# Performance work log

Hardware: AMD Instinct MI355X
Metric: run time of the kernel (lower is better)

The kernel has to match this reference:

```python
import jax, jax.numpy as jnp
import numpy as np

D_MODEL, N_HEADS, N_KV, HEAD_DIM, D_LAT = 1024, 8, 2, 128, 32
N_REP = N_HEADS // N_KV  # 4
B, T = 2, 2048


def setup_inputs() -> dict:
    key = jax.random.key(0)
    ks = jax.random.split(key, 8)
    s = lambda fan_in: 1.0 / np.sqrt(fan_in)
    return {
        "x": jax.random.normal(ks[0], (B, T, D_MODEL), jnp.float32),
        # weights stored as [in, out] (transpose of torch Linear.weight)
        "wq": jax.random.normal(ks[1], (D_MODEL, N_HEADS * HEAD_DIM), jnp.float32) * s(D_MODEL),
        "wk_down": jax.random.normal(ks[2], (D_MODEL, N_KV * D_LAT), jnp.float32) * s(D_MODEL),
        "wv_down": jax.random.normal(ks[3], (D_MODEL, N_KV * D_LAT), jnp.float32) * s(D_MODEL),
        "wk_up": jax.random.normal(ks[4], (D_LAT, HEAD_DIM), jnp.float32) * s(D_LAT),
        "wv_up": jax.random.normal(ks[5], (D_LAT, HEAD_DIM), jnp.float32) * s(D_LAT),
        "wo": jax.random.normal(ks[6], (N_HEADS * HEAD_DIM, D_MODEL), jnp.float32) * s(N_HEADS * HEAD_DIM),
    }


def reference(x, wq, wk_down, wv_down, wk_up, wv_up, wo):
    Bq, Tq, _ = x.shape
    scale = HEAD_DIM ** -0.5  # SDPA default scale
    # Q: [B,T,Hkv,Rep,Dh] (grouped view avoids materializing repeated K/V)
    q = (x @ wq).reshape(Bq, Tq, N_KV, N_REP, HEAD_DIM)
    # latent KV: [B,T,Hkv,Dl] -> up-project to [B,T,Hkv,Dh]
    k_lat = (x @ wk_down).reshape(Bq, Tq, N_KV, D_LAT)
    v_lat = (x @ wv_down).reshape(Bq, Tq, N_KV, D_LAT)
    k = jnp.einsum("bkhl,ld->bkhd", k_lat, wk_up)
    v = jnp.einsum("bkhl,ld->bkhd", v_lat, wv_up)
    # causal attention, GQA via grouped einsum (no repeat_interleave copy)
    scores = jnp.einsum("bqhrd,bkhd->bhrqk", q, k) * scale  # [B,Hkv,Rep,T,T]
    causal = jnp.tril(jnp.ones((Tq, Tq), dtype=bool))
    scores = jnp.where(causal, scores, jnp.finfo(scores.dtype).min)
    probs = jax.nn.softmax(scores, axis=-1)
    y = jnp.einsum("bhrqk,bkhd->bqhrd", probs, v)  # [B,T,Hkv,Rep,Dh]
    y = y.reshape(Bq, Tq, N_HEADS * HEAD_DIM)
    return y @ wo
```

## Files before the change

### kernel.cpp

```cpp
#include <hip/hip_runtime.h>
#include <hip/hip_bf16.h>


typedef __bf16 bf16_t;
typedef bf16_t bf16x8 __attribute__((ext_vector_type(8)));
typedef float f32x4 __attribute__((ext_vector_type(4)));

__device__ inline bf16x8 cvt8(const float* __restrict__ p) {
  f32x4 a = *(const f32x4*)p, b = *(const f32x4*)(p + 4);
  bf16x8 r;
#pragma unroll
  for (int i = 0; i < 4; ++i) { r[i] = (bf16_t)a[i]; r[4 + i] = (bf16_t)b[i]; }
  return r;
}

__global__ __launch_bounds__(256) void prep_mfma(
    const float* __restrict__ wq, const float* __restrict__ wkd,
    const float* __restrict__ wvd, const float* __restrict__ wku,
    const float* __restrict__ wvu, const float* __restrict__ wo,
    bf16_t* __restrict__ WqkvT, bf16_t* __restrict__ WcombT) {
  __shared__ __align__(16) char smem[34816];
  const int tid = threadIdx.x;
  const int wave = tid >> 6, lane = tid & 63;
  const int quad = lane >> 4, col = lane & 15;
  const int bi = blockIdx.x;

  if (bi < 64) {
    const int h = bi >> 3;
    const int c0 = (bi & 7) * 128 + wave * 32;
    f32x4 acc[2][2];
#pragma unroll
    for (int i = 0; i < 2; ++i)
#pragma unroll
      for (int j = 0; j < 2; ++j) acc[i][j] = (f32x4){0.f, 0.f, 0.f, 0.f};
#pragma unroll
    for (int ks = 0; ks < 4; ++ks) {
      const int ko = ks * 32 + quad * 8;
      bf16x8 a0 = cvt8(wku + col * 128 + ko);
      bf16x8 a1 = cvt8(wku + (16 + col) * 128 + ko);
      bf16x8 b0 = cvt8(wq + (size_t)(c0 + col) * 1024 + h * 128 + ko);
      bf16x8 b1 = cvt8(wq + (size_t)(c0 + 16 + col) * 1024 + h * 128 + ko);
      acc[0][0] = __builtin_amdgcn_mfma_f32_16x16x32_bf16(a0, b0, acc[0][0], 0, 0, 0);
      acc[0][1] = __builtin_amdgcn_mfma_f32_16x16x32_bf16(a0, b1, acc[0][1], 0, 0, 0);
      acc[1][0] = __builtin_amdgcn_mfma_f32_16x16x32_bf16(a1, b0, acc[1][0], 0, 0, 0);
      acc[1][1] = __builtin_amdgcn_mfma_f32_16x16x32_bf16(a1, b1, acc[1][1], 0, 0, 0);
    }
#pragma unroll
    for (int ms = 0; ms < 2; ++ms)
#pragma unroll
      for (int ns = 0; ns < 2; ++ns)
#pragma unroll
        for (int v = 0; v < 4; ++v)
          WqkvT[(size_t)(h * 32 + ms * 16 + quad * 4 + v) * 1024 + c0 + ns * 16 + col] =
              (bf16_t)acc[ms][ns][v];
  } else if (bi < 128) {
    const int b2 = bi - 64;
    const int h = b2 >> 3, m0 = (b2 & 7) * 128;
    bf16_t(*B_lds)[136] = (bf16_t(*)[136])smem;
    {
      const int d = tid >> 1, mh = (tid & 1) * 64;
      const float* wp = wo + (size_t)(h * 128 + d) * 1024 + m0 + mh;
#pragma unroll
      for (int i = 0; i < 16; ++i) {
        f32x4 w4 = *(const f32x4*)(wp + i * 4);
#pragma unroll
        for (int t = 0; t < 4; ++t) B_lds[mh + i * 4 + t][d] = (bf16_t)w4[t];
      }
    }
    __syncthreads();
    f32x4 acc[2][2];
#pragma unroll
    for (int i = 0; i < 2; ++i)
#pragma unroll
      for (int j = 0; j < 2; ++j) acc[i][j] = (f32x4){0.f, 0.f, 0.f, 0.f};
#pragma unroll
    for (int ks = 0; ks < 4; ++ks) {
      const int ko = ks * 32 + quad * 8;
      bf16x8 a0 = cvt8(wvu + col * 128 + ko);
      bf16x8 a1 = cvt8(wvu + (16 + col) * 128 + ko);
      bf16x8 b0 = *(const bf16x8*)&B_lds[wave * 32 + col][ko];
      bf16x8 b1 = *(const bf16x8*)&B_lds[wave * 32 + 16 + col][ko];
      acc[0][0] = __builtin_amdgcn_mfma_f32_16x16x32_bf16(a0, b0, acc[0][0], 0, 0, 0);
      acc[0][1] = __builtin_amdgcn_mfma_f32_16x16x32_bf16(a0, b1, acc[0][1], 0, 0, 0);
      acc[1][0] = __builtin_amdgcn_mfma_f32_16x16x32_bf16(a1, b0, acc[1][0], 0, 0, 0);
      acc[1][1] = __builtin_amdgcn_mfma_f32_16x16x32_bf16(a1, b1, acc[1][1], 0, 0, 0);
    }
#pragma unroll
    for (int ms = 0; ms < 2; ++ms)
#pragma unroll
      for (int ns = 0; ns < 2; ++ns)
#pragma unroll
        for (int v = 0; v < 4; ++v)
          WcombT[(size_t)(m0 + wave * 32 + ns * 16 + col) * 256 +
                 h * 32 + ms * 16 + quad * 4 + v] = (bf16_t)acc[ms][ns][v];
  } else {
    const int b3 = bi - 128;
    const int mat = b3 >> 4, c0 = (b3 & 15) * 64;
    const float* in = mat ? wvd : wkd;
    bf16_t(*tT)[72] = (bf16_t(*)[72])smem;
    {
      const int cc = tid >> 2, jq = (tid & 3) * 16;
      const float* ip = in + (size_t)(c0 + cc) * 64 + jq;
#pragma unroll
      for (int q = 0; q < 4; ++q) {
        f32x4 v4 = *(const f32x4*)(ip + q * 4);
#pragma unroll
        for (int t = 0; t < 4; ++t) tT[jq + q * 4 + t][cc] = (bf16_t)v4[t];
      }
    }
    __syncthreads();
    {
      const int j = tid >> 2, cq = (tid & 3) * 16;
      bf16_t* op = WqkvT + (size_t)(256 + mat * 64 + j) * 1024 + c0 + cq;
      *(bf16x8*)op = *(const bf16x8*)&tT[j][cq];
      *(bf16x8*)(op + 8) = *(const bf16x8*)&tT[j][cq + 8];
    }
  }
}

__global__ __launch_bounds__(256) void gemm_qkv(
    const float* __restrict__ A, const bf16_t* __restrict__ Bt,
    bf16_t* __restrict__ C) {
  __shared__ bf16_t As[32][72];
  __shared__ bf16_t Bs[128][72];
  const int tid = threadIdx.x;
  const int wave = tid >> 6, lane = tid & 63;
  const int quad = lane >> 4, col = lane & 15;
  const int wm = (wave >> 1) * 16, wn = (wave & 1) * 64;
  const int m0 = blockIdx.y * 32, n0 = blockIdx.x * 128;

  f32x4 acc[4];
#pragma unroll
  for (int j = 0; j < 4; ++j) acc[j] = (f32x4){0.f, 0.f, 0.f, 0.f};

  const int ar = tid >> 3, ac = (tid & 7) * 8;
  const int br = tid >> 1, bc = (tid & 1) * 32;
  const float* aP = A + (size_t)(m0 + ar) * 1024 + ac;
  const bf16_t* bP = Bt + (size_t)(n0 + br) * 1024 + bc;

  bf16x8 aR0 = cvt8(aP);
  bf16x8 bR0 = *(const bf16x8*)bP, bR1 = *(const bf16x8*)(bP + 8);
  bf16x8 bR2 = *(const bf16x8*)(bP + 16), bR3 = *(const bf16x8*)(bP + 24);

  for (int kt = 0; kt < 16; ++kt) {
    *(bf16x8*)&As[ar][ac] = aR0;
    *(bf16x8*)&Bs[br][bc] = bR0; *(bf16x8*)&Bs[br][bc + 8] = bR1;
    *(bf16x8*)&Bs[br][bc + 16] = bR2; *(bf16x8*)&Bs[br][bc + 24] = bR3;
    __syncthreads();
    if (kt < 15) {
      const int k0 = (kt + 1) * 64;
      aR0 = cvt8(aP + k0);
      bR0 = *(const bf16x8*)(bP + k0); bR1 = *(const bf16x8*)(bP + k0 + 8);
      bR2 = *(const bf16x8*)(bP + k0 + 16); bR3 = *(const bf16x8*)(bP + k0 + 24);
    }
#pragma unroll
    for (int ks = 0; ks < 2; ++ks) {
      bf16x8 af = *(const bf16x8*)&As[wm + col][ks * 32 + quad * 8];
      bf16x8 bfr[4];
#pragma unroll
      for (int j = 0; j < 4; ++j) bfr[j] = *(const bf16x8*)&Bs[wn + j * 16 + col][ks * 32 + quad * 8];
#pragma unroll
      for (int j = 0; j < 4; ++j)
        acc[j] = __builtin_amdgcn_mfma_f32_16x16x32_bf16(af, bfr[j], acc[j], 0, 0, 0);
    }
    __syncthreads();
  }

#pragma unroll
  for (int j = 0; j < 4; ++j) {
    const int cg = n0 + wn + j * 16 + col;
#pragma unroll
    for (int v = 0; v < 4; ++v)
      C[(size_t)(m0 + wm + quad * 4 + v) * 384 + cg] = (bf16_t)acc[j][v];
  }
}

__global__ __launch_bounds__(256) void gemm_out(
    const bf16_t* __restrict__ A, const bf16_t* __restrict__ Bt,
    float* __restrict__ C) {
  __shared__ bf16_t As[64][72];
  __shared__ bf16_t Bs[128][72];
  const int tid = threadIdx.x;
  const int wave = tid >> 6, lane = tid & 63;
  const int quad = lane >> 4, col = lane & 15;
  const int wm = (wave >> 1) * 32, wn = (wave & 1) * 64;
  const int m0 = blockIdx.y * 64, n0 = blockIdx.x * 128;

  f32x4 acc[2][4];
#pragma unroll
  for (int i = 0; i < 2; ++i)
#pragma unroll
    for (int j = 0; j < 4; ++j) acc[i][j] = (f32x4){0.f, 0.f, 0.f, 0.f};

  const int ar = tid >> 2, ac = (tid & 3) * 16;
  const int br = tid >> 1, bc = (tid & 1) * 32;
  const bf16_t* aP = A + (size_t)(m0 + ar) * 384 + ac;
  const bf16_t* bP = Bt + (size_t)(n0 + br) * 256 + bc;

  bf16x8 aR0 = *(const bf16x8*)aP, aR1 = *(const bf16x8*)(aP + 8);
  bf16x8 bR0 = *(const bf16x8*)bP, bR1 = *(const bf16x8*)(bP + 8);
  bf16x8 bR2 = *(const bf16x8*)(bP + 16), bR3 = *(const bf16x8*)(bP + 24);

  for (int kt = 0; kt < 4; ++kt) {
    *(bf16x8*)&As[ar][ac] = aR0; *(bf16x8*)&As[ar][ac + 8] = aR1;
    *(bf16x8*)&Bs[br][bc] = bR0; *(bf16x8*)&Bs[br][bc + 8] = bR1;
    *(bf16x8*)&Bs[br][bc + 16] = bR2; *(bf16x8*)&Bs[br][bc + 24] = bR3;
    __syncthreads();
    if (kt < 3) {
      const int k0 = (kt + 1) * 64;
      aR0 = *(const bf16x8*)(aP + k0); aR1 = *(const bf16x8*)(aP + k0 + 8);
      bR0 = *(const bf16x8*)(bP + k0); bR1 = *(const bf16x8*)(bP + k0 + 8);
      bR2 = *(const bf16x8*)(bP + k0 + 16); bR3 = *(const bf16x8*)(bP + k0 + 24);
    }
#pragma unroll
    for (int ks = 0; ks < 2; ++ks) {
      bf16x8 af[2], bfr[4];
#pragma unroll
      for (int i = 0; i < 2; ++i) af[i] = *(const bf16x8*)&As[wm + i * 16 + col][ks * 32 + quad * 8];
#pragma unroll
      for (int j = 0; j < 4; ++j) bfr[j] = *(const bf16x8*)&Bs[wn + j * 16 + col][ks * 32 + quad * 8];
#pragma unroll
      for (int i = 0; i < 2; ++i)
#pragma unroll
        for (int j = 0; j < 4; ++j)
          acc[i][j] = __builtin_amdgcn_mfma_f32_16x16x32_bf16(af[i], bfr[j], acc[i][j], 0, 0, 0);
    }
    __syncthreads();
  }

#pragma unroll
  for (int i = 0; i < 2; ++i) {
    const int rg = m0 + wm + i * 16 + quad * 4;
#pragma unroll
    for (int j = 0; j < 4; ++j) {
      const int cg = n0 + wn + j * 16 + col;
#pragma unroll
      for (int v = 0; v < 4; ++v)
        C[(size_t)(rg + v) * 1024 + cg] = acc[i][j][v];
    }
  }
}

__global__ __launch_bounds__(256) void attn_lat(bf16_t* QKV) {
  const int bi = blockIdx.x;
  const int half = bi >> 8, rest = bi & 255;
  const int qt = half ? 127 - (rest >> 1) : (rest >> 1);
  const int hkv = rest & 1, b = half;
  const int tid = threadIdx.x;
  const int wave = tid >> 6, lane = tid & 63;
  const int quad = lane >> 4, col = lane & 15;

  __shared__ bf16_t Ks[2][128][40];
  __shared__ bf16_t Vt[2][32][136];
  __shared__ bf16_t Ps[4][16][136];

  const int qb = qt * 16;
  const size_t rowbase = (size_t)b * 2048;
  const int qcol0 = (hkv * 4 + wave) * 32;

  bf16x8 a_q = *(const bf16x8*)(QKV + (rowbase + qb + col) * 384 + qcol0 + quad * 8);

  f32x4 o0 = (f32x4){0.f, 0.f, 0.f, 0.f};
  f32x4 o1 = (f32x4){0.f, 0.f, 0.f, 0.f};
  float lsum[4] = {0.f, 0.f, 0.f, 0.f};

  const int nkt = (qb >> 7) + 1;
  const float scale = 0.08838834764831843f;

  const int kr = tid >> 1, dc = (tid & 1) * 16;
  const bf16_t* kvBase = QKV + (rowbase + kr) * 384 + 256 + hkv * 32 + dc;

  {
    bf16x8 kA = *(const bf16x8*)kvBase, kB = *(const bf16x8*)(kvBase + 8);
    bf16x8 vA = *(const bf16x8*)(kvBase + 64), vB = *(const bf16x8*)(kvBase + 72);
    *(bf16x8*)&Ks[0][kr][dc] = kA;
    *(bf16x8*)&Ks[0][kr][dc + 8] = kB;
#pragma unroll
    for (int t = 0; t < 8; ++t) { Vt[0][dc + t][kr] = vA[t]; Vt[0][dc + 8 + t][kr] = vB[t]; }
  }
  __syncthreads();

  for (int kt = 0; kt < nkt; ++kt) {
    const int cur = kt & 1;
    const int kb = kt * 128;
    const bool more = (kt + 1 < nkt);

    bf16x8 kA, kB, vA, vB;
    if (more) {
      const bf16_t* np = kvBase + (size_t)(kt + 1) * 128 * 384;
      kA = *(const bf16x8*)np; kB = *(const bf16x8*)(np + 8);
      vA = *(const bf16x8*)(np + 64); vB = *(const bf16x8*)(np + 72);
    }

    f32x4 s[8];
#pragma unroll
    for (int k8 = 0; k8 < 8; ++k8) {
      bf16x8 bk = *(const bf16x8*)&Ks[cur][k8 * 16 + col][quad * 8];
      s[k8] = __builtin_amdgcn_mfma_f32_16x16x32_bf16(a_q, bk, (f32x4){0.f, 0.f, 0.f, 0.f}, 0, 0, 0);
    }

    const bool full = (kb + 128 <= qb);
#pragma unroll
    for (int v = 0; v < 4; ++v) {
      const int qr = quad * 4 + v;
      const int qg = qb + qr;
#pragma unroll
      for (int k8 = 0; k8 < 8; ++k8) {
        float xx = s[k8][v] * scale;
        if (!full && (kb + k8 * 16 + col > qg)) xx = -1e30f;
        const float p = __expf(xx);
        lsum[v] += p;
        Ps[wave][qr][k8 * 16 + col] = (bf16_t)p;
      }
    }
    __asm__ __volatile__("" ::: "memory");

#pragma unroll
    for (int kc = 0; kc < 4; ++kc) {
      bf16x8 a_p = *(const bf16x8*)&Ps[wave][col][kc * 32 + quad * 8];
      bf16x8 bv0 = *(const bf16x8*)&Vt[cur][col][kc * 32 + quad * 8];
      bf16x8 bv1 = *(const bf16x8*)&Vt[cur][16 + col][kc * 32 + quad * 8];
      o0 = __builtin_amdgcn_mfma_f32_16x16x32_bf16(a_p, bv0, o0, 0, 0, 0);
      o1 = __builtin_amdgcn_mfma_f32_16x16x32_bf16(a_p, bv1, o1, 0, 0, 0);
    }

    if (more) {
      *(bf16x8*)&Ks[cur ^ 1][kr][dc] = kA;
      *(bf16x8*)&Ks[cur ^ 1][kr][dc + 8] = kB;
#pragma unroll
      for (int t = 0; t < 8; ++t) { Vt[cur ^ 1][dc + t][kr] = vA[t]; Vt[cur ^ 1][dc + 8 + t][kr] = vB[t]; }
    }
    __syncthreads();
  }

#pragma unroll
  for (int v = 0; v < 4; ++v) {
    float l = lsum[v];
#pragma unroll
    for (int off = 8; off; off >>= 1) l += __shfl_xor(l, off, 64);
    const float inv = 1.f / l;
    const size_t r = (rowbase + qb + quad * 4 + v) * 384 + qcol0;
    QKV[r + col] = (bf16_t)(o0[v] * inv);
    QKV[r + 16 + col] = (bf16_t)(o1[v] * inv);
  }
}

extern "C" void kernel_launch(void* const* d_in, const int* in_sizes, int n_in,
                              void* d_out, int out_size, void* d_ws, size_t ws_size,
                              hipStream_t stream) {
  (void)in_sizes; (void)n_in; (void)out_size; (void)ws_size;
  const float* x   = (const float*)d_in[0];
  const float* wq  = (const float*)d_in[1];
  const float* wkd = (const float*)d_in[2];
  const float* wvd = (const float*)d_in[3];
  const float* wku = (const float*)d_in[4];
  const float* wvu = (const float*)d_in[5];
  const float* wo  = (const float*)d_in[6];
  float* out = (float*)d_out;

  bf16_t* WqkvT  = (bf16_t*)d_ws;
  bf16_t* WcombT = WqkvT + (size_t)384 * 1024;
  bf16_t* QKV    = WcombT + (size_t)1024 * 256;

  prep_mfma<<<160, 256, 0, stream>>>(wq, wkd, wvd, wku, wvu, wo, WqkvT, WcombT);
  gemm_qkv<<<dim3(3, 128), 256, 0, stream>>>(x, WqkvT, QKV);
  attn_lat<<<512, 256, 0, stream>>>(QKV);
  gemm_out<<<dim3(8, 64), 256, 0, stream>>>(QKV, WcombT, out);
}
```

Before: 139.0 us.

## Pre-convert x to bf16 in prep kernel, shrink attention LDS padding, add occupancy hint

The prep kernel gains 128 extra blocks that convert x from fp32 to bf16 into workspace, so gemm_qkv reads bf16 A directly instead of re-reading and converting fp32 x for each of its 3 column tiles. Separately, attn_lat's LDS row padding is reduced and a min-blocks-per-CU of 3 is added to the launch bounds to raise occupancy. The conversion costs an extra write and read of x, and the new padding may change LDS bank conflicts.

```diff
diff --git a/kernel.cpp b/kernel.cpp
--- a/kernel.cpp
+++ b/kernel.cpp
@@ -15,9 +15,10 @@
 }
 
 __global__ __launch_bounds__(256) void prep_mfma(
-    const float* __restrict__ wq, const float* __restrict__ wkd,
-    const float* __restrict__ wvd, const float* __restrict__ wku,
-    const float* __restrict__ wvu, const float* __restrict__ wo,
+    const float* __restrict__ x, const float* __restrict__ wq,
+    const float* __restrict__ wkd, const float* __restrict__ wvd,
+    const float* __restrict__ wku, const float* __restrict__ wvu,
+    const float* __restrict__ wo, bf16_t* __restrict__ Xb,
     bf16_t* __restrict__ WqkvT, bf16_t* __restrict__ WcombT) {
   __shared__ __align__(16) char smem[34816];
   const int tid = threadIdx.x;
@@ -93,7 +94,7 @@
         for (int v = 0; v < 4; ++v)
           WcombT[(size_t)(m0 + wave * 32 + ns * 16 + col) * 256 +
                  h * 32 + ms * 16 + quad * 4 + v] = (bf16_t)acc[ms][ns][v];
-  } else {
+  } else if (bi < 160) {
     const int b3 = bi - 128;
     const int mat = b3 >> 4, c0 = (b3 & 15) * 64;
     const float* in = mat ? wvd : wkd;
@@ -115,11 +116,20 @@
       *(bf16x8*)op = *(const bf16x8*)&tT[j][cq];
       *(bf16x8*)(op + 8) = *(const bf16x8*)&tT[j][cq + 8];
     }
+  } else {
+    const size_t base = (size_t)(bi - 160) * 32768;
+    const float* ip = x + base;
+    bf16_t* op = Xb + base;
+#pragma unroll
+    for (int it = 0; it < 16; ++it) {
+      const int o = it * 2048 + tid * 8;
+      *(bf16x8*)(op + o) = cvt8(ip + o);
+    }
   }
 }
 
 __global__ __launch_bounds__(256) void gemm_qkv(
-    const float* __restrict__ A, const bf16_t* __restrict__ Bt,
+    const bf16_t* __restrict__ A, const bf16_t* __restrict__ Bt,
     bf16_t* __restrict__ C) {
   __shared__ bf16_t As[32][72];
   __shared__ bf16_t Bs[128][72];
@@ -135,10 +145,10 @@
 
   const int ar = tid >> 3, ac = (tid & 7) * 8;
   const int br = tid >> 1, bc = (tid & 1) * 32;
-  const float* aP = A + (size_t)(m0 + ar) * 1024 + ac;
+  const bf16_t* aP = A + (size_t)(m0 + ar) * 1024 + ac;
   const bf16_t* bP = Bt + (size_t)(n0 + br) * 1024 + bc;
 
-  bf16x8 aR0 = cvt8(aP);
+  bf16x8 aR0 = *(const bf16x8*)aP;
   bf16x8 bR0 = *(const bf16x8*)bP, bR1 = *(const bf16x8*)(bP + 8);
   bf16x8 bR2 = *(const bf16x8*)(bP + 16), bR3 = *(const bf16x8*)(bP + 24);
 
@@ -149,7 +159,7 @@
     __syncthreads();
     if (kt < 15) {
       const int k0 = (kt + 1) * 64;
-      aR0 = cvt8(aP + k0);
+      aR0 = *(const bf16x8*)(aP + k0);
       bR0 = *(const bf16x8*)(bP + k0); bR1 = *(const bf16x8*)(bP + k0 + 8);
       bR2 = *(const bf16x8*)(bP + k0 + 16); bR3 = *(const bf16x8*)(bP + k0 + 24);
     }
@@ -241,7 +251,7 @@
   }
 }
 
-__global__ __launch_bounds__(256) void attn_lat(bf16_t* QKV) {
+__global__ __launch_bounds__(256, 3) void attn_lat(bf16_t* QKV) {
   const int bi = blockIdx.x;
   const int half = bi >> 8, rest = bi & 255;
   const int qt = half ? 127 - (rest >> 1) : (rest >> 1);
@@ -250,9 +260,9 @@
   const int wave = tid >> 6, lane = tid & 63;
   const int quad = lane >> 4, col = lane & 15;
 
-  __shared__ bf16_t Ks[2][128][40];
-  __shared__ bf16_t Vt[2][32][136];
-  __shared__ bf16_t Ps[4][16][136];
+  __shared__ bf16_t Ks[2][128][36];
+  __shared__ bf16_t Vt[2][32][132];
+  __shared__ bf16_t Ps[4][16][132];
 
   const int qb = qt * 16;
   const size_t rowbase = (size_t)b * 2048;
@@ -361,9 +371,10 @@
   bf16_t* WqkvT  = (bf16_t*)d_ws;
   bf16_t* WcombT = WqkvT + (size_t)384 * 1024;
   bf16_t* QKV    = WcombT + (size_t)1024 * 256;
-
-  prep_mfma<<<160, 256, 0, stream>>>(wq, wkd, wvd, wku, wvu, wo, WqkvT, WcombT);
-  gemm_qkv<<<dim3(3, 128), 256, 0, stream>>>(x, WqkvT, QKV);
+  bf16_t* Xb     = QKV + (size_t)4096 * 384;
+
+  prep_mfma<<<288, 256, 0, stream>>>(x, wq, wkd, wvd, wku, wvu, wo, Xb, WqkvT, WcombT);
+  gemm_qkv<<<dim3(3, 128), 256, 0, stream>>>(Xb, WqkvT, QKV);
   attn_lat<<<512, 256, 0, stream>>>(QKV);
   gemm_out<<<dim3(8, 64), 256, 0, stream>>>(QKV, WcombT, out);
 }
```

Measured after the change: 137.3 us. About the same (-1.2%).
